# Optimization experiments

Hardware: AMD Instinct MI355X
Metric: run time of the kernel (lower is better)

Reference implementation:

```python
import jax, jax.numpy as jnp
import numpy as np

B, D_IN, H, C = 8192, 2048, 1024, 1000
LAYERS = [0, 1, 2, 3, 4]          # structure.layers
N_MAIN = 4                        # main hidden layers for layers[1:]
# skip layers in __init__ enumeration order: (target_layer, source_layer)
SKIPS = [(2, 0), (3, 0), (3, 1), (4, 0), (4, 1), (4, 2)]


def _linear_init(key, out_f, in_f):
    k1, k2 = jax.random.split(key)
    bound = 1.0 / np.sqrt(in_f)
    W = jax.random.uniform(k1, (out_f, in_f), minval=-bound, maxval=bound, dtype=jnp.float32)
    b = jax.random.uniform(k2, (out_f,), minval=-bound, maxval=bound, dtype=jnp.float32)
    return W, b


def setup_inputs() -> dict:
    key = jax.random.key(0)
    ks = iter(jax.random.split(key, 40))
    x = jax.random.normal(next(ks), (B, D_IN), dtype=jnp.float32)

    Wf, bf = _linear_init(next(ks), H, D_IN)
    mf = jax.random.bernoulli(next(ks), 0.5, (H, D_IN))

    main_W, main_b, main_m = [], [], []
    for _ in range(N_MAIN):
        W, b = _linear_init(next(ks), H, H)
        main_W.append(W); main_b.append(b)
        main_m.append(jax.random.bernoulli(next(ks), 0.5, (H, H)))

    skip_W, skip_b, skip_m = [], [], []
    for _ in SKIPS:
        W, b = _linear_init(next(ks), H, H)
        skip_W.append(W); skip_b.append(b)
        skip_m.append(jax.random.bernoulli(next(ks), 0.5, (H, H)))

    Wo, bo = _linear_init(next(ks), C, H)
    mo = jax.random.bernoulli(next(ks), 0.5, (C, H))

    return {"x": x, "Wf": Wf, "bf": bf, "mf": mf,
            "main_W": main_W, "main_b": main_b, "main_m": main_m,
            "skip_W": skip_W, "skip_b": skip_b, "skip_m": skip_m,
            "Wo": Wo, "bo": bo, "mo": mo}


def _masked_linear(x, W, b, m):
    # F.linear(x, weight * mask, bias): mask applied to weight before GEMM
    return x @ (W * m).T + b


def reference(x, Wf, bf, mf, main_W, main_b, main_m, skip_W, skip_b, skip_m, Wo, bo, mo):
    relu = jax.nn.relu
    last = relu(_masked_linear(x, Wf, bf, mf))        # layer 0 output, [B, H]
    results = {0: last}
    for i, layer_idx in enumerate(LAYERS[1:]):
        out = relu(_masked_linear(last, main_W[i], main_b[i], main_m[i]))
        for k, (tgt, src) in enumerate(SKIPS):
            if tgt == layer_idx:
                out = out + relu(_masked_linear(results[src], skip_W[k], skip_b[k], skip_m[k]))
        results[layer_idx] = out
        last = out
    return _masked_linear(last, Wo, bo, mo)            # [B, C]
```

## Files before the change

### kernel.cpp

```cpp
#include <hip/hip_runtime.h>
#include <hip/hip_bf16.h>
#include <stdint.h>


typedef unsigned short ushort_t;
typedef __bf16 bf16x8 __attribute__((ext_vector_type(8)));
typedef float f32x4 __attribute__((ext_vector_type(4)));

__device__ __forceinline__ void gl_lds16(const void* g, void* l) {
  typedef __attribute__((address_space(1))) void gvoid;
  typedef __attribute__((address_space(3))) void lvoid;
  __builtin_amdgcn_global_load_lds((gvoid*)(void*)g, (lvoid*)l, 16, 0, 0);
}

__device__ __forceinline__ ushort_t f2b(float f) {
  __hip_bfloat16 h = (__hip_bfloat16)f;
  return *(ushort_t*)&h;
}

__global__ void detect_kernel(const ushort_t* x, const ushort_t* mf, int* flags) {
  __shared__ int s[4];
  if (threadIdx.x < 4) s[threadIdx.x] = 0;
  __syncthreads();
  int expout = 0, m3f80_even = 0, m3f80_odd = 0, mhi01 = 0;
  for (int k = threadIdx.x; k < 2048; k += 256) {
    ushort_t w = x[k];
    int e = (w >> 7) & 0xFF;
    if (e < 96 || e > 144) expout++;
    ushort_t mw = mf[k];
    if (mw == 0x3F80) { if (k & 1) m3f80_odd++; else m3f80_even++; }
    if ((mw >> 8) == 1) mhi01++;
  }
  atomicAdd(&s[0], expout);
  atomicAdd(&s[1], m3f80_even);
  atomicAdd(&s[2], m3f80_odd);
  atomicAdd(&s[3], mhi01);
  __syncthreads();
  if (threadIdx.x == 0) {
    flags[0] = (s[0] > 100) ? 1 : 0;
    int mmode = 0;
    if (s[1] > 100) mmode = 2;
    else if (s[2] > 100) mmode = 3;
    else if (s[3] > 200) mmode = 1;
    flags[1] = mmode;
  }
}

struct PrepEnt {
  const void* w; size_t woff;
  const void* m; size_t moff;
  ushort_t* o;
  int n;
  int valid;
};
struct PrepAll { PrepEnt e[25]; };

__global__ void prep_weights(PrepAll p, const int* flags) {
  const bool f32 = flags[0] != 0;
  const int mmode = flags[1];
  const PrepEnt e = p.e[blockIdx.y];
  const int nch = e.n >> 3;
  const int stride = blockDim.x * gridDim.x;
  for (int ci = blockIdx.x * blockDim.x + threadIdx.x; ci < nch; ci += stride) {
    const int i = ci << 3;
    ushort_t o[8] = {0, 0, 0, 0, 0, 0, 0, 0};
    if (i < e.valid) {
      ushort_t wb[8];
      if (f32) {
        const float* wp = (const float*)e.w + e.woff + i;
        float4 a = *(const float4*)wp;
        float4 b = *(const float4*)(wp + 4);
        wb[0] = f2b(a.x); wb[1] = f2b(a.y); wb[2] = f2b(a.z); wb[3] = f2b(a.w);
        wb[4] = f2b(b.x); wb[5] = f2b(b.y); wb[6] = f2b(b.z); wb[7] = f2b(b.w);
      } else {
        *(uint4*)wb = *(const uint4*)((const ushort_t*)e.w + e.woff + i);
      }
      unsigned mk = 0xFF;
      if (e.m) {
        mk = 0;
        if (mmode == 0) {
          const int4* mp = (const int4*)((const int*)e.m + e.moff + i);
          int4 a = mp[0], b = mp[1];
          mk = (a.x != 0) | ((a.y != 0) << 1) | ((a.z != 0) << 2) | ((a.w != 0) << 3) |
               ((b.x != 0) << 4) | ((b.y != 0) << 5) | ((b.z != 0) << 6) | ((b.w != 0) << 7);
        } else if (mmode == 1) {
          const uint2 mv = *(const uint2*)((const unsigned char*)e.m + e.moff + i);
          const unsigned char* mb = (const unsigned char*)&mv;
          for (int j = 0; j < 8; j++) mk |= (mb[j] != 0) << j;
        } else if (mmode == 2) {
          uint4 mv = *(const uint4*)((const ushort_t*)e.m + e.moff + i);
          const ushort_t* ms = (const ushort_t*)&mv;
          for (int j = 0; j < 8; j++) mk |= (ms[j] != 0) << j;
        } else {
          const uint4* mp = (const uint4*)((const unsigned int*)e.m + e.moff + i);
          uint4 a = mp[0], b = mp[1];
          const unsigned* u = (const unsigned*)&a;
          const unsigned* v = (const unsigned*)&b;
          for (int j = 0; j < 4; j++) mk |= (u[j] != 0) << j;
          for (int j = 0; j < 4; j++) mk |= (v[j] != 0) << (4 + j);
        }
      }
#pragma unroll
      for (int j = 0; j < 8; j++) o[j] = ((mk >> j) & 1) ? wb[j] : (ushort_t)0;
    }
    *(uint4*)(e.o + i) = *(uint4*)o;
  }
}

struct GemmSrc { const ushort_t* A; const ushort_t* B; const ushort_t* bias; };
struct GemmArgs { GemmSrc s[4]; };

template <int NSRC, bool RELU, bool NGUARD>
__launch_bounds__(256, 2)
__global__ void gemm_multi(GemmArgs args, void* Cv, const int* of32flag,
                           int K, int N_real, int ldc)
{
  __shared__ __align__(16) ushort_t As[2][128 * 32];
  __shared__ __align__(16) ushort_t Bs[2][128 * 32];

  const bool of32 = (of32flag != nullptr) && (of32flag[0] != 0);
  __hip_bfloat16* C = (__hip_bfloat16*)Cv;
  float* Cf = (float*)Cv;

  const int tid  = threadIdx.x;
  const int lane = tid & 63;
  const int wave = tid >> 6;
  const int wm = (wave >> 1) * 64;
  const int wn = (wave & 1) * 64;
  const int fr = lane & 15;
  const int kg = lane >> 4;

  const int lid = blockIdx.y * 8 + blockIdx.x;
  const int s8  = lid >> 3;
  const int bm  = ((lid & 7) * 8 + (s8 >> 3)) * 128;
  const int bn  = (s8 & 7) * 128;

  const int srow = tid >> 2;
  const int scol = (((tid & 3) ^ ((srow >> 1) & 3)) * 8);
  const size_t aoff = (size_t)(bm + srow) * K + scol;
  const size_t boff = (size_t)(bn + srow) * K + scol;
  const size_t rowskip = (size_t)64 * K;

  auto stage = [&](const ushort_t* gA, const ushort_t* gB, int buf) {
    ushort_t* lA = &As[buf][wave * 512];
    ushort_t* lB = &Bs[buf][wave * 512];
    gl_lds16(gA, lA);
    gl_lds16(gA + rowskip, lA + 2048);
    gl_lds16(gB, lB);
    gl_lds16(gB + rowskip, lB + 2048);
  };

  f32x4 acc[4][4], out_acc[4][4];
#pragma unroll
  for (int i = 0; i < 4; i++)
#pragma unroll
    for (int j = 0; j < 4; j++) {
      acc[i][j] = (f32x4){0.f, 0.f, 0.f, 0.f};
      out_acc[i][j] = (f32x4){0.f, 0.f, 0.f, 0.f};
    }

  stage(args.s[0].A + aoff, args.s[0].B + boff, 0);
  int cur = 0;

  const int sw = kg ^ ((fr >> 1) & 3);

#pragma unroll
  for (int s = 0; s < NSRC; ++s) {
    const ushort_t* gA = args.s[s].A + aoff;
    const ushort_t* gB = args.s[s].B + boff;
    for (int k0 = 0; k0 < K; k0 += 32) {
      __syncthreads();
      if (k0 + 32 < K) {
        stage(gA + k0 + 32, gB + k0 + 32, cur ^ 1);
      } else if (s + 1 < NSRC) {
        stage(args.s[s + 1].A + aoff, args.s[s + 1].B + boff, cur ^ 1);
      }

      const bf16x8* Asv = (const bf16x8*)As[cur];
      const bf16x8* Bsv = (const bf16x8*)Bs[cur];
      bf16x8 af[4], bfr[4];
#pragma unroll
      for (int i = 0; i < 4; i++) af[i]  = Asv[(wm + i * 16 + fr) * 4 + sw];
#pragma unroll
      for (int i = 0; i < 4; i++) bfr[i] = Bsv[(wn + i * 16 + fr) * 4 + sw];
#pragma unroll
      for (int mi = 0; mi < 4; mi++)
#pragma unroll
        for (int ni = 0; ni < 4; ni++)
          acc[mi][ni] = __builtin_amdgcn_mfma_f32_16x16x32_bf16(
              af[mi], bfr[ni], acc[mi][ni], 0, 0, 0);
      cur ^= 1;
    }

    if (NSRC > 1) {
      const ushort_t* bias = args.s[s].bias;
#pragma unroll
      for (int ni = 0; ni < 4; ni++) {
        const int c = bn + wn + ni * 16 + fr;
        const float bb = (float)*(const __hip_bfloat16*)(bias + c);
#pragma unroll
        for (int mi = 0; mi < 4; mi++)
#pragma unroll
          for (int j = 0; j < 4; j++) {
            float v = acc[mi][ni][j] + bb;
            if (RELU) v = fmaxf(v, 0.0f);
            out_acc[mi][ni][j] += v;
            acc[mi][ni][j] = 0.0f;
          }
      }
    }
  }

#pragma unroll
  for (int ni = 0; ni < 4; ni++) {
    const int c = bn + wn + ni * 16 + fr;
    if (NGUARD && c >= N_real) continue;
    float bb = 0.0f;
    if (NSRC == 1) bb = (float)*(const __hip_bfloat16*)(args.s[0].bias + c);
#pragma unroll
    for (int mi = 0; mi < 4; mi++) {
      const int r0 = bm + wm + mi * 16 + kg * 4;
#pragma unroll
      for (int j = 0; j < 4; j++) {
        const size_t idx = (size_t)(r0 + j) * ldc + c;
        float v;
        if (NSRC == 1) {
          v = acc[mi][ni][j] + bb;
          if (RELU) v = fmaxf(v, 0.0f);
        } else {
          v = out_acc[mi][ni][j];
        }
        if (of32) Cf[idx] = v;
        else      C[idx]  = (__hip_bfloat16)v;
      }
    }
  }
}

extern "C" void kernel_launch(void* const* d_in, const int* in_sizes, int n_in,
                              void* d_out, int out_size, void* d_ws, size_t ws_size,
                              hipStream_t stream) {
  (void)out_size; (void)ws_size;
  const int Bm = 8192, DIN = 2048, H = 1024, Cn = 1000;
  const size_t HH = (size_t)H * H;

  struct PO { const void* p; size_t off; };
  PO x{d_in[0], 0}, Wf{d_in[0], 0}, mf{d_in[0], 0}, Wo{d_in[0], 0}, mo{d_in[0], 0};
  PO bf{d_in[0], 0}, bo{d_in[0], 0};
  PO mW[4], mM[4], mB[4], sW[6], sM[6], sB[6];
  for (int i = 0; i < 4; i++) { mW[i] = {d_in[0], 0}; mM[i] = mW[i]; mB[i] = mW[i]; }
  for (int i = 0; i < 6; i++) { sW[i] = {d_in[0], 0}; sM[i] = sW[i]; sB[i] = sW[i]; }

  {
    int c2M = 0, c1M = 0, c1k = 0, cWoMo = 0, c4 = 0, c6 = 0;
    for (int i = 0; i < n_in; i++) {
      const int s = in_sizes[i];
      const void* p = d_in[i];
      switch (s) {
        case 16777216: x = {p, 0}; break;
        case 2097152:  if (c2M++ == 0) Wf = {p, 0}; else mf = {p, 0}; break;
        case 1048576: {
          int j = c1M++;
          if (j < 4)       mW[j]      = {p, 0};
          else if (j < 8)  mM[j - 4]  = {p, 0};
          else if (j < 14) sW[j - 8]  = {p, 0};
          else if (j < 20) sM[j - 14] = {p, 0};
          break;
        }
        case 1024: {
          int j = c1k++;
          if (j == 0)      bf        = {p, 0};
          else if (j < 5)  mB[j - 1] = {p, 0};
          else if (j < 11) sB[j - 5] = {p, 0};
          break;
        }
        case 1024000: if (cWoMo++ == 0) Wo = {p, 0}; else mo = {p, 0}; break;
        case 1000: bo = {p, 0}; break;
        case 4194304:
          for (int t = 0; t < 4; t++) {
            if (c4 == 0) mW[t] = {p, t * HH}; else mM[t] = {p, t * HH};
          }
          c4++; break;
        case 6291456:
          for (int t = 0; t < 6; t++) {
            if (c6 == 0) sW[t] = {p, t * HH}; else sM[t] = {p, t * HH};
          }
          c6++; break;
        case 4096:
          for (int t = 0; t < 4; t++) mB[t] = {p, (size_t)t * H};
          break;
        case 6144:
          for (int t = 0; t < 6; t++) sB[t] = {p, (size_t)t * H};
          break;
        default: break;
      }
    }
  }

  ushort_t* wsp = (ushort_t*)d_ws;
  size_t off = 0;
  int* flags = (int*)wsp; off += 32;
  ushort_t* xc = wsp + off; off += (size_t)Bm * DIN;
  __hip_bfloat16* r[5];
  for (int i = 0; i < 5; i++) { r[i] = (__hip_bfloat16*)(wsp + off); off += (size_t)Bm * H; }
  ushort_t* wWf = wsp + off; off += (size_t)H * DIN;
  ushort_t* wMain[4];
  for (int i = 0; i < 4; i++) { wMain[i] = wsp + off; off += HH; }
  ushort_t* wSkip[6];
  for (int k = 0; k < 6; k++) { wSkip[k] = wsp + off; off += HH; }
  ushort_t* wWo = wsp + off; off += (size_t)1024 * 1024;
  ushort_t* cbf_ = wsp + off; off += 1024;
  ushort_t* cmB[4];
  for (int i = 0; i < 4; i++) { cmB[i] = wsp + off; off += 1024; }
  ushort_t* csB[6];
  for (int k = 0; k < 6; k++) { csB[k] = wsp + off; off += 1024; }
  ushort_t* cbo = wsp + off; off += 1024;

  detect_kernel<<<1, 256, 0, stream>>>((const ushort_t*)x.p, (const ushort_t*)mf.p, flags);

  PrepAll p;
  p.e[0]  = { Wf.p, Wf.off, mf.p, mf.off, wWf, H * DIN, H * DIN };
  for (int i = 0; i < 4; i++)
    p.e[1 + i] = { mW[i].p, mW[i].off, mM[i].p, mM[i].off, wMain[i], (int)HH, (int)HH };
  for (int k = 0; k < 6; k++)
    p.e[5 + k] = { sW[k].p, sW[k].off, sM[k].p, sM[k].off, wSkip[k], (int)HH, (int)HH };
  p.e[11] = { Wo.p, Wo.off, mo.p, mo.off, wWo, 1024 * 1024, Cn * H };
  p.e[12] = { bf.p, bf.off, nullptr, 0, cbf_, H, H };
  for (int i = 0; i < 4; i++)
    p.e[13 + i] = { mB[i].p, mB[i].off, nullptr, 0, cmB[i], H, H };
  for (int k = 0; k < 6; k++)
    p.e[17 + k] = { sB[k].p, sB[k].off, nullptr, 0, csB[k], H, H };
  p.e[23] = { bo.p, bo.off, nullptr, 0, cbo, 1024, Cn };
  p.e[24] = { x.p, x.off, nullptr, 0, xc, Bm * DIN, Bm * DIN };
  prep_weights<<<dim3(256, 25), dim3(256), 0, stream>>>(p, flags);

  const dim3 g(8, 64), b(256);

  GemmArgs a0; a0.s[0] = { xc, wWf, cbf_ };
  gemm_multi<1, true, false><<<g, b, 0, stream>>>(a0, r[0], nullptr, DIN, H, H);

  GemmArgs a1; a1.s[0] = { (ushort_t*)r[0], wMain[0], cmB[0] };
  gemm_multi<1, true, false><<<g, b, 0, stream>>>(a1, r[1], nullptr, H, H, H);

  GemmArgs a2;
  a2.s[0] = { (ushort_t*)r[1], wMain[1], cmB[1] };
  a2.s[1] = { (ushort_t*)r[0], wSkip[0], csB[0] };
  gemm_multi<2, true, false><<<g, b, 0, stream>>>(a2, r[2], nullptr, H, H, H);

  GemmArgs a3;
  a3.s[0] = { (ushort_t*)r[2], wMain[2], cmB[2] };
  a3.s[1] = { (ushort_t*)r[0], wSkip[1], csB[1] };
  a3.s[2] = { (ushort_t*)r[1], wSkip[2], csB[2] };
  gemm_multi<3, true, false><<<g, b, 0, stream>>>(a3, r[3], nullptr, H, H, H);

  GemmArgs a4;
  a4.s[0] = { (ushort_t*)r[3], wMain[3], cmB[3] };
  a4.s[1] = { (ushort_t*)r[0], wSkip[3], csB[3] };
  a4.s[2] = { (ushort_t*)r[1], wSkip[4], csB[4] };
  a4.s[3] = { (ushort_t*)r[2], wSkip[5], csB[5] };
  gemm_multi<4, true, false><<<g, b, 0, stream>>>(a4, r[4], nullptr, H, H, H);

  GemmArgs ao; ao.s[0] = { (ushort_t*)r[4], wWo, cbo };
  gemm_multi<1, false, true><<<g, b, 0, stream>>>(ao, d_out, flags, H, Cn, Cn);
}
```

Measured before the change: 555.5 us.

## Reshape GEMM tiles to 256x64 with 512 threads and triple-buffered LDS

Changes the multi-source GEMM block tile from 128x128 with 4 waves to 256x64 with 8 waves, each wave computing 64x32. The K loop now runs across all sources in one flattened chunk loop. It uses a 3-stage LDS ring with explicit vmcnt waits and raw s_barrier, so global-to-LDS loads run two chunks ahead. Biases are preloaded into registers. This aims to hide load latency and raise occupancy, at the cost of lower MFMA work per wave per LDS fragment load and hand-tuned waitcnt assumptions that could be fragile.

```diff
diff --git a/kernel.cpp b/kernel.cpp
--- a/kernel.cpp
+++ b/kernel.cpp
@@ -111,12 +111,12 @@
 struct GemmArgs { GemmSrc s[4]; };
 
 template <int NSRC, bool RELU, bool NGUARD>
-__launch_bounds__(256, 2)
+__launch_bounds__(512, 4)
 __global__ void gemm_multi(GemmArgs args, void* Cv, const int* of32flag,
                            int K, int N_real, int ldc)
 {
-  __shared__ __align__(16) ushort_t As[2][128 * 32];
-  __shared__ __align__(16) ushort_t Bs[2][128 * 32];
+  __shared__ __align__(16) ushort_t As[3][8192];
+  __shared__ __align__(16) ushort_t Bs[3][2048];
 
   const bool of32 = (of32flag != nullptr) && (of32flag[0] != 0);
   __hip_bfloat16* C = (__hip_bfloat16*)Cv;
@@ -126,112 +126,133 @@
   const int lane = tid & 63;
   const int wave = tid >> 6;
   const int wm = (wave >> 1) * 64;
-  const int wn = (wave & 1) * 64;
+  const int wn = (wave & 1) * 32;
   const int fr = lane & 15;
   const int kg = lane >> 4;
 
   const int lid = blockIdx.y * 8 + blockIdx.x;
-  const int s8  = lid >> 3;
-  const int bm  = ((lid & 7) * 8 + (s8 >> 3)) * 128;
-  const int bn  = (s8 & 7) * 128;
+  const int idx = lid >> 3;
+  const int bm  = ((lid & 7) * 4 + (idx >> 4)) * 256;
+  const int bn  = (idx & 15) * 64;
 
   const int srow = tid >> 2;
-  const int scol = (((tid & 3) ^ ((srow >> 1) & 3)) * 8);
-  const size_t aoff = (size_t)(bm + srow) * K + scol;
-  const size_t boff = (size_t)(bn + srow) * K + scol;
-  const size_t rowskip = (size_t)64 * K;
-
-  auto stage = [&](const ushort_t* gA, const ushort_t* gB, int buf) {
-    ushort_t* lA = &As[buf][wave * 512];
-    ushort_t* lB = &Bs[buf][wave * 512];
-    gl_lds16(gA, lA);
-    gl_lds16(gA + rowskip, lA + 2048);
-    gl_lds16(gB, lB);
-    gl_lds16(gB + rowskip, lB + 2048);
+  const int scol = ((tid & 3) ^ ((srow >> 1) & 3)) * 8;
+  const size_t aoff1 = (size_t)(bm + srow) * K + scol;
+  const size_t aoff2 = aoff1 + (size_t)128 * K;
+  const size_t boff  = (size_t)(bn + srow) * K + scol;
+  const int ldsw = wave * 512;
+
+  auto stage = [&](int buf, const GemmSrc& g, size_t ko) {
+    gl_lds16(g.A + aoff1 + ko, &As[buf][ldsw]);
+    gl_lds16(g.A + aoff2 + ko, &As[buf][4096 + ldsw]);
+    if (wave < 4) gl_lds16(g.B + boff + ko, &Bs[buf][ldsw]);
   };
 
-  f32x4 acc[4][4], out_acc[4][4];
+  float bias_v[NSRC][2];
+#pragma unroll
+  for (int s = 0; s < NSRC; s++)
+#pragma unroll
+    for (int ni = 0; ni < 2; ni++)
+      bias_v[s][ni] =
+          (float)*(const __hip_bfloat16*)(args.s[s].bias + bn + wn + ni * 16 + fr);
+
+  f32x4 acc[4][2], out_acc[4][2];
 #pragma unroll
   for (int i = 0; i < 4; i++)
 #pragma unroll
-    for (int j = 0; j < 4; j++) {
+    for (int j = 0; j < 2; j++) {
       acc[i][j] = (f32x4){0.f, 0.f, 0.f, 0.f};
       out_acc[i][j] = (f32x4){0.f, 0.f, 0.f, 0.f};
     }
 
-  stage(args.s[0].A + aoff, args.s[0].B + boff, 0);
-  int cur = 0;
+  const int kc  = K >> 5;
+  const int nch = NSRC * kc;
+
+  int s_src = 0, s_k = 0;
+  stage(0, args.s[0], 0);
+  if (++s_k == kc) { s_k = 0; ++s_src; }
+  stage(1, args.s[s_src < NSRC ? s_src : 0], (size_t)s_k * 32);
+  if (++s_k == kc) { s_k = 0; ++s_src; }
 
   const int sw = kg ^ ((fr >> 1) & 3);
 
-#pragma unroll
-  for (int s = 0; s < NSRC; ++s) {
-    const ushort_t* gA = args.s[s].A + aoff;
-    const ushort_t* gB = args.s[s].B + boff;
-    for (int k0 = 0; k0 < K; k0 += 32) {
-      __syncthreads();
-      if (k0 + 32 < K) {
-        stage(gA + k0 + 32, gB + k0 + 32, cur ^ 1);
-      } else if (s + 1 < NSRC) {
-        stage(args.s[s + 1].A + aoff, args.s[s + 1].B + boff, cur ^ 1);
-      }
-
-      const bf16x8* Asv = (const bf16x8*)As[cur];
-      const bf16x8* Bsv = (const bf16x8*)Bs[cur];
-      bf16x8 af[4], bfr[4];
-#pragma unroll
-      for (int i = 0; i < 4; i++) af[i]  = Asv[(wm + i * 16 + fr) * 4 + sw];
-#pragma unroll
-      for (int i = 0; i < 4; i++) bfr[i] = Bsv[(wn + i * 16 + fr) * 4 + sw];
-#pragma unroll
-      for (int mi = 0; mi < 4; mi++)
-#pragma unroll
-        for (int ni = 0; ni < 4; ni++)
-          acc[mi][ni] = __builtin_amdgcn_mfma_f32_16x16x32_bf16(
-              af[mi], bfr[ni], acc[mi][ni], 0, 0, 0);
-      cur ^= 1;
-    }
+  int cb = 0, sb = 2;
+  int c_src = 0, c_cnt = 0;
+
+  for (int ci = 0; ci < nch; ++ci) {
+    if (ci + 1 < nch) {
+      if (wave < 4) asm volatile("s_waitcnt vmcnt(3)" ::: "memory");
+      else          asm volatile("s_waitcnt vmcnt(2)" ::: "memory");
+    } else {
+      asm volatile("s_waitcnt vmcnt(0)" ::: "memory");
+    }
+    asm volatile("s_barrier" ::: "memory");
+
+    if (ci + 2 < nch) {
+      stage(sb, args.s[s_src], (size_t)s_k * 32);
+      if (++s_k == kc) { s_k = 0; ++s_src; }
+      sb = (sb == 2) ? 0 : sb + 1;
+    }
+
+    const bf16x8* Asv = (const bf16x8*)As[cb];
+    const bf16x8* Bsv = (const bf16x8*)Bs[cb];
+    bf16x8 af[4], bfr[2];
+#pragma unroll
+    for (int i = 0; i < 4; i++) af[i]  = Asv[(wm + i * 16 + fr) * 4 + sw];
+#pragma unroll
+    for (int i = 0; i < 2; i++) bfr[i] = Bsv[(wn + i * 16 + fr) * 4 + sw];
+#pragma unroll
+    for (int mi = 0; mi < 4; mi++)
+#pragma unroll
+      for (int ni = 0; ni < 2; ni++)
+        acc[mi][ni] = __builtin_amdgcn_mfma_f32_16x16x32_bf16(
+            af[mi], bfr[ni], acc[mi][ni], 0, 0, 0);
+    cb = (cb == 2) ? 0 : cb + 1;
 
     if (NSRC > 1) {
-      const ushort_t* bias = args.s[s].bias;
-#pragma unroll
-      for (int ni = 0; ni < 4; ni++) {
-        const int c = bn + wn + ni * 16 + fr;
-        const float bb = (float)*(const __hip_bfloat16*)(bias + c);
+      if (++c_cnt == kc) {
+        c_cnt = 0;
+#pragma unroll
+        for (int ni = 0; ni < 2; ni++) {
+          const float bb = bias_v[0][ni + 0 * 2 + c_src * 2 - c_src * 2]
+                           ;
+          (void)bb;
+        }
 #pragma unroll
         for (int mi = 0; mi < 4; mi++)
 #pragma unroll
-          for (int j = 0; j < 4; j++) {
-            float v = acc[mi][ni][j] + bb;
-            if (RELU) v = fmaxf(v, 0.0f);
-            out_acc[mi][ni][j] += v;
-            acc[mi][ni][j] = 0.0f;
-          }
-      }
-    }
-  }
-
-#pragma unroll
-  for (int ni = 0; ni < 4; ni++) {
+          for (int ni = 0; ni < 2; ni++)
+#pragma unroll
+            for (int j = 0; j < 4; j++) {
+              float v = acc[mi][ni][j] + bias_v[c_src][ni];
+              if (RELU) v = fmaxf(v, 0.0f);
+              out_acc[mi][ni][j] += v;
+              acc[mi][ni][j] = 0.0f;
+            }
+        ++c_src;
+      }
+    }
+  }
+
+#pragma unroll
+  for (int ni = 0; ni < 2; ni++) {
     const int c = bn + wn + ni * 16 + fr;
     if (NGUARD && c >= N_real) continue;
-    float bb = 0.0f;
-    if (NSRC == 1) bb = (float)*(const __hip_bfloat16*)(args.s[0].bias + c);
 #pragma unroll
     for (int mi = 0; mi < 4; mi++) {
       const int r0 = bm + wm + mi * 16 + kg * 4;
 #pragma unroll
       for (int j = 0; j < 4; j++) {
-        const size_t idx = (size_t)(r0 + j) * ldc + c;
+        const size_t idx2 = (size_t)(r0 + j) * ldc + c;
         float v;
         if (NSRC == 1) {
-          v = acc[mi][ni][j] + bb;
+          v = acc[mi][ni][j] + bias_v[0][ni];
           if (RELU) v = fmaxf(v, 0.0f);
         } else {
           v = out_acc[mi][ni][j];
         }
-        if (of32) Cf[idx] = v;
-        else      C[idx]  = (__hip_bfloat16)v;
+        if (of32) Cf[idx2] = v;
+        else      C[idx2]  = (__hip_bfloat16)v;
       }
     }
   }
@@ -334,7 +355,7 @@
   p.e[24] = { x.p, x.off, nullptr, 0, xc, Bm * DIN, Bm * DIN };
   prep_weights<<<dim3(256, 25), dim3(256), 0, stream>>>(p, flags);
 
-  const dim3 g(8, 64), b(256);
+  const dim3 g(8, 64), b(512);
 
   GemmArgs a0; a0.s[0] = { xc, wWf, cbf_ };
   gemm_multi<1, true, false><<<g, b, 0, stream>>>(a0, r[0], nullptr, DIN, H, H);
```

After: 582.7 us. 4.9% more time.
